# Optimization experiments

Hardware: AMD Instinct MI355X
Metric: run time of the kernel (lower is better)

Reference implementation:

```python
import jax, jax.numpy as jnp
import numpy as np

N, K, F, H, C = 16384, 16, 3, 64, 10


def setup_inputs() -> dict:
    key = jax.random.key(0)
    ks = jax.random.split(key, 6)
    pos = jax.random.normal(ks[0], (N, F), jnp.float32)
    batch = jnp.zeros((N,), jnp.int32)  # single graph
    W1 = jax.random.normal(ks[1], (2 * F, H), jnp.float32) * 0.1
    b1 = jnp.zeros((H,), jnp.float32)
    W2 = jax.random.normal(ks[2], (2 * H, H), jnp.float32) * 0.1
    b2 = jnp.zeros((H,), jnp.float32)
    Wc = jax.random.normal(ks[3], (H, C), jnp.float32) * 0.1
    bc = jnp.zeros((C,), jnp.float32)
    return {"pos": pos, "batch": batch, "W1": W1, "b1": b1,
            "W2": W2, "b2": b2, "Wc": Wc, "bc": bc}


def knn_graph(pos, k):
    # brute-force knn with self-loops (loop=True): self has distance 0
    sq = jnp.sum(pos * pos, axis=1)
    d = sq[:, None] + sq[None, :] - 2.0 * (pos @ pos.T)  # [N, N]
    _, idx = jax.lax.top_k(-d, k)  # [N, k] nearest neighbor indices (incl. self)
    return idx


def edge_conv(x, idx, W, b):
    # message for edge j->i: Linear(concat(x_i, x_j - x_i)); aggregate by max over neighbors
    n, k = idx.shape
    xi = x[:, None, :]               # [N, 1, F]
    xj = x[idx]                      # [N, k, F]
    msg = jnp.concatenate([jnp.broadcast_to(xi, (n, k, x.shape[1])), xj - xi], axis=-1)
    m = msg @ W + b                  # [N, k, H]
    return jnp.max(m, axis=1)        # [N, H]


def reference(pos, batch, W1, b1, W2, b2, Wc, bc):
    idx = knn_graph(pos, K)
    h = jax.nn.relu(edge_conv(pos, idx, W1, b1))
    h = jax.nn.relu(edge_conv(h, idx, W2, b2))
    g = jax.ops.segment_max(h, batch, num_segments=1)  # global max pool -> [1, H]
    return g @ Wc + bc
```

## Files before the change

### kernel.cpp

```cpp
#include <hip/hip_runtime.h>

#define NPTS 16384
#define KNN 16
#define HID 64
#define NCLS 10

#define CHUNKS_T 16
#define CHUNK_T (NPTS / CHUNKS_T)
#define NSTR 16
#define CHUNKS_S 32
#define CHUNK_S (NPTS / CHUNKS_S)
#define CAPS 12

__device__ __forceinline__ float distf(float4 q, float4 p) {
    float dot = fmaf(q.x, p.x, fmaf(q.y, p.y, q.z * p.z));
    return fmaf(-2.f, dot, p.w);
}

__device__ __forceinline__ unsigned long long dkey(float v, int j) {
    unsigned u = __float_as_uint(v);
    u = (u & 0x80000000u) ? ~u : (u | 0x80000000u);
    return ((unsigned long long)u << 32) | (unsigned)j;
}

__device__ __forceinline__ unsigned long long shfl_xor_u64(unsigned long long x, int m) {
    unsigned hi = (unsigned)__shfl_xor((int)(x >> 32), m, 64);
    unsigned lo = (unsigned)__shfl_xor((int)(x & 0xffffffffu), m, 64);
    return ((unsigned long long)hi << 32) | lo;
}

template <int NS>
__device__ __forceinline__ void wave_top16(unsigned long long (&key)[NS], int lane,
                                           int q, int* __restrict__ idx) {
    int outj = 0x7fffffff;
    for (int r = 0; r < 16; ++r) {
        unsigned long long gm = key[0];
#pragma unroll
        for (int s = 1; s < NS; ++s) gm = key[s] < gm ? key[s] : gm;
#pragma unroll
        for (int st = 1; st < 64; st <<= 1) {
            unsigned long long o = shfl_xor_u64(gm, st);
            gm = o < gm ? o : gm;
        }
        if (lane == r) outj = (int)(gm & 0xffffffffu);
#pragma unroll
        for (int s = 0; s < NS; ++s)
            if (key[s] == gm) key[s] = ~0ull;
    }
    if (lane < 16) idx[q * KNN + lane] = outj;
}

__global__ void prep_kernel(const float* __restrict__ pos, float4* __restrict__ pos4) {
    int i = blockIdx.x * 256 + threadIdx.x;
    if (i < NPTS) {
        float x = pos[3 * i], y = pos[3 * i + 1], z = pos[3 * i + 2];
        pos4[i] = make_float4(x, y, z, fmaf(x, x, fmaf(y, y, z * z)));
    }
}

__global__ __launch_bounds__(256) void knn_tau_kernel(const float4* __restrict__ pos4,
                                                      float* __restrict__ minpart) {
    int tid = threadIdx.x;
    int q0 = blockIdx.x * 512 + tid;
    int q1 = q0 + 256;
    int c = blockIdx.y;
    float4 qa = pos4[q0];
    float4 qb = pos4[q1];
    float mna[NSTR], mnb[NSTR];
#pragma unroll
    for (int u = 0; u < NSTR; ++u) { mna[u] = INFINITY; mnb[u] = INFINITY; }
    __shared__ float4 tile[256];
    int base = c * CHUNK_T;
    for (int t0 = 0; t0 < CHUNK_T; t0 += 256) {
        __syncthreads();
        tile[tid] = pos4[base + t0 + tid];
        __syncthreads();
        for (int jj = 0; jj < 256; jj += NSTR) {
#pragma unroll
            for (int u = 0; u < NSTR; ++u) {
                float4 p = tile[jj + u];
                mna[u] = fminf(mna[u], distf(qa, p));
                mnb[u] = fminf(mnb[u], distf(qb, p));
            }
        }
    }
#pragma unroll
    for (int u = 0; u < NSTR; ++u) {
        minpart[(c * NSTR + u) * NPTS + q0] = mna[u];
        minpart[(c * NSTR + u) * NPTS + q1] = mnb[u];
    }
}

__global__ __launch_bounds__(256) void knn_tau_reduce_kernel(const float* __restrict__ minpart,
                                                             float* __restrict__ tau) {
    int q = blockIdx.x * 256 + threadIdx.x;
    float t = -INFINITY;
#pragma unroll
    for (int u = 0; u < NSTR; ++u) {
        float m = INFINITY;
#pragma unroll
        for (int c = 0; c < CHUNKS_T; ++c) m = fminf(m, minpart[(c * NSTR + u) * NPTS + q]);
        t = fmaxf(t, m);
    }
    tau[q] = t;
}

__global__ __launch_bounds__(256) void knn_survey_kernel(const float4* __restrict__ pos4,
                                                         const float* __restrict__ tau,
                                                         int* __restrict__ surv,
                                                         int* __restrict__ cnt,
                                                         int* __restrict__ flags) {
    int tid = threadIdx.x;
    int q0 = blockIdx.x * 512 + tid;
    int q1 = q0 + 256;
    int c = blockIdx.y;
    float4 qa = pos4[q0], qb = pos4[q1];
    float ta = tau[q0], tb = tau[q1];
    __shared__ float4 tile[256];
    int base = c * CHUNK_S;
    int ca = 0, cb = 0;
    int sba = (q0 * CHUNKS_S + c) * CAPS;
    int sbb = (q1 * CHUNKS_S + c) * CAPS;
    for (int t0 = 0; t0 < CHUNK_S; t0 += 256) {
        __syncthreads();
        tile[tid] = pos4[base + t0 + tid];
        __syncthreads();
#pragma unroll 4
        for (int jj = 0; jj < 256; ++jj) {
            float4 p = tile[jj];
            int j = base + t0 + jj;
            float va = distf(qa, p);
            float vb = distf(qb, p);
            if (va <= ta) { if (ca < CAPS) surv[sba + ca] = j; ++ca; }
            if (vb <= tb) { if (cb < CAPS) surv[sbb + cb] = j; ++cb; }
        }
    }
    cnt[q0 * CHUNKS_S + c] = ca;
    cnt[q1 * CHUNKS_S + c] = cb;
    if (ca > CAPS) flags[q0] = 1;
    if (cb > CAPS) flags[q1] = 1;
}

__global__ __launch_bounds__(256) void knn_final_kernel(const float4* __restrict__ pos4,
                                                        const int* __restrict__ surv,
                                                        const int* __restrict__ cnt,
                                                        const int* __restrict__ flags,
                                                        const float* __restrict__ tau,
                                                        int* __restrict__ idx) {
    __shared__ unsigned long long buf[4][CHUNKS_S * CAPS];
    __shared__ int nbuf[4];
    int lane = threadIdx.x & 63;
    int w = threadIdx.x >> 6;
    int q = blockIdx.x * 4 + w;
    float4 qp = pos4[q];
    if (lane == 0) nbuf[w] = 0;
    if (flags[q] == 0) {
        int c = lane & 31;
        int sb = lane >> 5;
        int n = min(cnt[q * CHUNKS_S + c], CAPS);
        int sbase = (q * CHUNKS_S + c) * CAPS;
        int nv = n - sb;
        int nk = nv > 0 ? (nv + 1) >> 1 : 0;
        unsigned long long key[6];
#pragma unroll
        for (int r = 0; r < 6; ++r) key[r] = ~0ull;
#pragma unroll
        for (int r = 0; r < 6; ++r) {
            if (r < nk) {
                int j = surv[sbase + sb + 2 * r];
                key[r] = dkey(distf(qp, pos4[j]), j);
            }
        }
        int pos = atomicAdd(&nbuf[w], nk);
#pragma unroll
        for (int r = 0; r < 6; ++r)
            if (r < nk) buf[w][pos + r] = key[r];
        int ntot = atomicAdd(&nbuf[w], 0);
        int rank[6];
#pragma unroll
        for (int r = 0; r < 6; ++r) rank[r] = 0;
        for (int t = 0; t < ntot; ++t) {
            unsigned long long k = buf[w][t];
#pragma unroll
            for (int r = 0; r < 6; ++r) rank[r] += (int)(r < nk && k < key[r]);
        }
#pragma unroll
        for (int r = 0; r < 6; ++r)
            if (r < nk && rank[r] < 16) idx[q * KNN + rank[r]] = (int)(key[r] & 0xffffffffu);
    } else {
        float tq = tau[q];
        unsigned long long key[16];
#pragma unroll
        for (int u = 0; u < 16; ++u) key[u] = ~0ull;
        for (int j = lane; j < NPTS; j += 64) {
            float v = distf(qp, pos4[j]);
            unsigned long long k = dkey(v, j);
            if (v <= tq && k < key[15]) {
#pragma unroll
                for (int s = 0; s < 16; ++s) {
                    unsigned long long mn = k < key[s] ? k : key[s];
                    unsigned long long mx = k < key[s] ? key[s] : k;
                    key[s] = mn;
                    k = mx;
                }
            }
        }
        wave_top16<16>(key, lane, q, idx);
    }
}


__global__ __launch_bounds__(256) void ec1_pre_kernel(const float4* __restrict__ pos4,
                                                      const float* __restrict__ W1,
                                                      const float* __restrict__ b1,
                                                      float* __restrict__ C1,
                                                      float* __restrict__ Y1) {
    int t = threadIdx.x & 63;
    int p = blockIdx.x * 4 + (threadIdx.x >> 6);
    float4 x = pos4[p];
    float w0 = W1[0 * HID + t], w1 = W1[1 * HID + t], w2 = W1[2 * HID + t];
    float v0 = W1[3 * HID + t], v1 = W1[4 * HID + t], v2 = W1[5 * HID + t];
    float y = fmaf(x.x, v0, fmaf(x.y, v1, x.z * v2));
    float cc = b1[t] + x.x * (w0 - v0) + x.y * (w1 - v1) + x.z * (w2 - v2);
    Y1[p * HID + t] = y;
    C1[p * HID + t] = cc;
}

__global__ __launch_bounds__(256) void ec1_max_kernel(const float* __restrict__ C1,
                                                      const float* __restrict__ Y1,
                                                      const int* __restrict__ idx,
                                                      float* __restrict__ h1) {
    int t = threadIdx.x & 63;
    int p = blockIdx.x * 4 + (threadIdx.x >> 6);
    float m = -INFINITY;
#pragma unroll
    for (int k = 0; k < KNN; ++k) {
        int j = idx[p * KNN + k];
        m = fmaxf(m, Y1[j * HID + t]);
    }
    h1[p * HID + t] = fmaxf(C1[p * HID + t] + m, 0.f);
}

__global__ __launch_bounds__(256) void ec2_pre_kernel(const float* __restrict__ h1,
                                                      const float* __restrict__ W2,
                                                      const float* __restrict__ b2,
                                                      float* __restrict__ C2,
                                                      float* __restrict__ Y2) {
    int t = threadIdx.x & 63;
    int r = threadIdx.x >> 6;
    int pb = blockIdx.x * 16 + r * 4;
    float aa[4] = {0.f, 0.f, 0.f, 0.f};
    float ab[4] = {0.f, 0.f, 0.f, 0.f};
#pragma unroll 8
    for (int f = 0; f < 64; ++f) {
        float wa = W2[f * HID + t];
        float wb = W2[(64 + f) * HID + t];
#pragma unroll
        for (int i = 0; i < 4; ++i) {
            float h = h1[(pb + i) * HID + f];
            aa[i] = fmaf(h, wa, aa[i]);
            ab[i] = fmaf(h, wb, ab[i]);
        }
    }
    float bt = b2[t];
#pragma unroll
    for (int i = 0; i < 4; ++i) {
        C2[(pb + i) * HID + t] = bt + aa[i] - ab[i];
        Y2[(pb + i) * HID + t] = ab[i];
    }
}

__global__ __launch_bounds__(256) void ec2_maxpool_kernel(const float* __restrict__ C2,
                                                          const float* __restrict__ Y2,
                                                          const int* __restrict__ idx,
                                                          float* __restrict__ gpartial) {
    int t = threadIdx.x & 63;
    int lp = threadIdx.x >> 6;
    int p = blockIdx.x * 4 + lp;
    float m = -INFINITY;
#pragma unroll
    for (int k = 0; k < KNN; ++k) {
        int j = idx[p * KNN + k];
        m = fmaxf(m, Y2[j * HID + t]);
    }
    float val = fmaxf(C2[p * HID + t] + m, 0.f);
    __shared__ float red[4][64];
    red[lp][t] = val;
    __syncthreads();
    if (lp == 0) {
        float g = fmaxf(fmaxf(red[0][t], red[1][t]), fmaxf(red[2][t], red[3][t]));
        gpartial[blockIdx.x * 64 + t] = g;
    }
}

__global__ __launch_bounds__(256) void greduce2_kernel(const float* __restrict__ gpartial,
                                                       float* __restrict__ gp2) {
    __shared__ float red[4][64];
    int f = threadIdx.x & 63;
    int w = threadIdx.x >> 6;
    int r0 = blockIdx.x * 16 + w * 4;
    float m = -INFINITY;
#pragma unroll
    for (int r = 0; r < 4; ++r) m = fmaxf(m, gpartial[(r0 + r) * 64 + f]);
    red[w][f] = m;
    __syncthreads();
    if (w == 0)
        gp2[blockIdx.x * 64 + f] =
            fmaxf(fmaxf(red[0][f], red[1][f]), fmaxf(red[2][f], red[3][f]));
}

__global__ __launch_bounds__(256) void tail2_kernel(const float* __restrict__ gp2,
                                                    const float* __restrict__ Wc,
                                                    const float* __restrict__ bc,
                                                    float* __restrict__ out) {
    __shared__ float red[4][64];
    __shared__ float g[64];
    int f = threadIdx.x & 63;
    int w = threadIdx.x >> 6;
    float m = -INFINITY;
    for (int i = w; i < 256; i += 4) m = fmaxf(m, gp2[i * 64 + f]);
    red[w][f] = m;
    __syncthreads();
    if (w == 0) g[f] = fmaxf(fmaxf(red[0][f], red[1][f]), fmaxf(red[2][f], red[3][f]));
    __syncthreads();
    if (threadIdx.x < NCLS) {
        float a = bc[threadIdx.x];
#pragma unroll
        for (int h = 0; h < HID; ++h) a = fmaf(g[h], Wc[h * NCLS + threadIdx.x], a);
        out[threadIdx.x] = a;
    }
}

extern "C" void kernel_launch(void* const* d_in, const int* in_sizes, int n_in,
                              void* d_out, int out_size, void* d_ws, size_t ws_size,
                              hipStream_t stream) {
    const float* pos = (const float*)d_in[0];
    const float* W1 = (const float*)d_in[2];
    const float* b1 = (const float*)d_in[3];
    const float* W2 = (const float*)d_in[4];
    const float* b2 = (const float*)d_in[5];
    const float* Wc = (const float*)d_in[6];
    const float* bc = (const float*)d_in[7];
    float* out = (float*)d_out;

    char* ws = (char*)d_ws;
    size_t o = 0;
    auto alloc = [&](size_t bytes) { size_t r = o; o += (bytes + 255) & ~size_t(255); return r; };
    size_t sz_minp = (size_t)NPTS * CHUNKS_T * NSTR * 4;
    size_t sz_surv = (size_t)NPTS * CHUNKS_S * CAPS * 4;
    size_t o_pos4 = alloc((size_t)NPTS * 16);
    size_t o_shared = alloc(sz_minp > sz_surv ? sz_minp : sz_surv);
    size_t o_tau = alloc((size_t)NPTS * 4);
    size_t o_cnt = alloc((size_t)NPTS * CHUNKS_S * 4);
    size_t o_flag = alloc((size_t)NPTS * 4);
    size_t o_idx = alloc((size_t)NPTS * KNN * 4);
    size_t o_h1 = alloc((size_t)NPTS * HID * 4);
    size_t o_gp = alloc((size_t)(NPTS / 4) * HID * 4);
    size_t o_gp2 = alloc((size_t)256 * HID * 4);

    float4* pos4 = (float4*)(ws + o_pos4);
    float* minp = (float*)(ws + o_shared);
    int* surv = (int*)(ws + o_shared);
    size_t fm = (size_t)NPTS * HID * 4;
    float* C1 = (float*)(ws + o_shared + 0 * fm);
    float* Y1 = (float*)(ws + o_shared + 1 * fm);
    float* C2 = (float*)(ws + o_shared + 2 * fm);
    float* Y2 = (float*)(ws + o_shared + 3 * fm);
    float* tau = (float*)(ws + o_tau);
    int* cnt = (int*)(ws + o_cnt);
    int* flags = (int*)(ws + o_flag);
    int* idx = (int*)(ws + o_idx);
    float* h1 = (float*)(ws + o_h1);
    float* gp = (float*)(ws + o_gp);
    float* gp2 = (float*)(ws + o_gp2);

    hipMemsetAsync(flags, 0, (size_t)NPTS * 4, stream);

    prep_kernel<<<NPTS / 256, 256, 0, stream>>>(pos, pos4);
    knn_tau_kernel<<<dim3(NPTS / 512, CHUNKS_T), 256, 0, stream>>>(pos4, minp);
    knn_tau_reduce_kernel<<<NPTS / 256, 256, 0, stream>>>(minp, tau);
    knn_survey_kernel<<<dim3(NPTS / 512, CHUNKS_S), 256, 0, stream>>>(pos4, tau, surv, cnt, flags);
    knn_final_kernel<<<NPTS / 4, 256, 0, stream>>>(pos4, surv, cnt, flags, tau, idx);
    ec1_pre_kernel<<<NPTS / 4, 256, 0, stream>>>(pos4, W1, b1, C1, Y1);
    ec1_max_kernel<<<NPTS / 4, 256, 0, stream>>>(C1, Y1, idx, h1);
    ec2_pre_kernel<<<NPTS / 16, 256, 0, stream>>>(h1, W2, b2, C2, Y2);
    ec2_maxpool_kernel<<<NPTS / 4, 256, 0, stream>>>(C2, Y2, idx, gp);
    greduce2_kernel<<<256, 256, 0, stream>>>(gp, gp2);
    tail2_kernel<<<1, 256, 0, stream>>>(gp2, Wc, bc, out);
}
```

Measured before the change: 345.3 us.

## Store precomputed distance keys in survey and restructure survey chunking

The survey kernel now writes 64-bit distance/index keys for surviving candidates instead of bare indices, so the final kernel reads the keys directly rather than gathering neighbor positions and recomputing distances. Survey also moves to one query per thread with 16 chunks and a capacity of 16 per chunk, instead of two queries per thread with 32 chunks of capacity 12. The final kernel maps 16 chunks by 4 sub-lanes, each handling up to 4 keys. This doubles the bytes per survivor slot and changes the survey's per-thread work and grid shape. A larger per-chunk capacity may also send fewer queries to the slow fallback path.

```diff
diff --git a/kernel.cpp b/kernel.cpp
--- a/kernel.cpp
+++ b/kernel.cpp
@@ -8,9 +8,9 @@
 #define CHUNKS_T 16
 #define CHUNK_T (NPTS / CHUNKS_T)
 #define NSTR 16
-#define CHUNKS_S 32
+#define CHUNKS_S 16
 #define CHUNK_S (NPTS / CHUNKS_S)
-#define CAPS 12
+#define CAPS 16
 
 __device__ __forceinline__ float distf(float4 q, float4 p) {
     float dot = fmaf(q.x, p.x, fmaf(q.y, p.y, q.z * p.z));
@@ -107,42 +107,37 @@
 
 __global__ __launch_bounds__(256) void knn_survey_kernel(const float4* __restrict__ pos4,
                                                          const float* __restrict__ tau,
-                                                         int* __restrict__ surv,
+                                                         unsigned long long* __restrict__ surv,
                                                          int* __restrict__ cnt,
                                                          int* __restrict__ flags) {
     int tid = threadIdx.x;
-    int q0 = blockIdx.x * 512 + tid;
-    int q1 = q0 + 256;
+    int q = blockIdx.x * 256 + tid;
     int c = blockIdx.y;
-    float4 qa = pos4[q0], qb = pos4[q1];
-    float ta = tau[q0], tb = tau[q1];
+    float4 qp = pos4[q];
+    float tq = tau[q];
     __shared__ float4 tile[256];
     int base = c * CHUNK_S;
-    int ca = 0, cb = 0;
-    int sba = (q0 * CHUNKS_S + c) * CAPS;
-    int sbb = (q1 * CHUNKS_S + c) * CAPS;
+    int cr = 0;
+    int sbase = (q * CHUNKS_S + c) * CAPS;
     for (int t0 = 0; t0 < CHUNK_S; t0 += 256) {
         __syncthreads();
         tile[tid] = pos4[base + t0 + tid];
         __syncthreads();
 #pragma unroll 4
         for (int jj = 0; jj < 256; ++jj) {
-            float4 p = tile[jj];
-            int j = base + t0 + jj;
-            float va = distf(qa, p);
-            float vb = distf(qb, p);
-            if (va <= ta) { if (ca < CAPS) surv[sba + ca] = j; ++ca; }
-            if (vb <= tb) { if (cb < CAPS) surv[sbb + cb] = j; ++cb; }
-        }
-    }
-    cnt[q0 * CHUNKS_S + c] = ca;
-    cnt[q1 * CHUNKS_S + c] = cb;
-    if (ca > CAPS) flags[q0] = 1;
-    if (cb > CAPS) flags[q1] = 1;
+            float v = distf(qp, tile[jj]);
+            if (v <= tq) {
+                if (cr < CAPS) surv[sbase + cr] = dkey(v, base + t0 + jj);
+                ++cr;
+            }
+        }
+    }
+    cnt[q * CHUNKS_S + c] = cr;
+    if (cr > CAPS) flags[q] = 1;
 }
 
 __global__ __launch_bounds__(256) void knn_final_kernel(const float4* __restrict__ pos4,
-                                                        const int* __restrict__ surv,
+                                                        const unsigned long long* __restrict__ surv,
                                                         const int* __restrict__ cnt,
                                                         const int* __restrict__ flags,
                                                         const float* __restrict__ tau,
@@ -152,42 +147,36 @@
     int lane = threadIdx.x & 63;
     int w = threadIdx.x >> 6;
     int q = blockIdx.x * 4 + w;
-    float4 qp = pos4[q];
     if (lane == 0) nbuf[w] = 0;
     if (flags[q] == 0) {
-        int c = lane & 31;
-        int sb = lane >> 5;
+        int c = lane & 15;
+        int sb = lane >> 4;
         int n = min(cnt[q * CHUNKS_S + c], CAPS);
         int sbase = (q * CHUNKS_S + c) * CAPS;
         int nv = n - sb;
-        int nk = nv > 0 ? (nv + 1) >> 1 : 0;
-        unsigned long long key[6];
-#pragma unroll
-        for (int r = 0; r < 6; ++r) key[r] = ~0ull;
-#pragma unroll
-        for (int r = 0; r < 6; ++r) {
-            if (r < nk) {
-                int j = surv[sbase + sb + 2 * r];
-                key[r] = dkey(distf(qp, pos4[j]), j);
-            }
-        }
+        int nk = nv > 0 ? (nv + 3) >> 2 : 0;
+        unsigned long long key[4];
+#pragma unroll
+        for (int r = 0; r < 4; ++r)
+            key[r] = (r < nk) ? surv[sbase + sb + 4 * r] : ~0ull;
         int pos = atomicAdd(&nbuf[w], nk);
 #pragma unroll
-        for (int r = 0; r < 6; ++r)
+        for (int r = 0; r < 4; ++r)
             if (r < nk) buf[w][pos + r] = key[r];
         int ntot = atomicAdd(&nbuf[w], 0);
-        int rank[6];
-#pragma unroll
-        for (int r = 0; r < 6; ++r) rank[r] = 0;
+        int rank[4];
+#pragma unroll
+        for (int r = 0; r < 4; ++r) rank[r] = 0;
         for (int t = 0; t < ntot; ++t) {
             unsigned long long k = buf[w][t];
 #pragma unroll
-            for (int r = 0; r < 6; ++r) rank[r] += (int)(r < nk && k < key[r]);
-        }
-#pragma unroll
-        for (int r = 0; r < 6; ++r)
+            for (int r = 0; r < 4; ++r) rank[r] += (int)(r < nk && k < key[r]);
+        }
+#pragma unroll
+        for (int r = 0; r < 4; ++r)
             if (r < nk && rank[r] < 16) idx[q * KNN + rank[r]] = (int)(key[r] & 0xffffffffu);
     } else {
+        float4 qp = pos4[q];
         float tq = tau[q];
         unsigned long long key[16];
 #pragma unroll
@@ -347,7 +336,7 @@
     size_t o = 0;
     auto alloc = [&](size_t bytes) { size_t r = o; o += (bytes + 255) & ~size_t(255); return r; };
     size_t sz_minp = (size_t)NPTS * CHUNKS_T * NSTR * 4;
-    size_t sz_surv = (size_t)NPTS * CHUNKS_S * CAPS * 4;
+    size_t sz_surv = (size_t)NPTS * CHUNKS_S * CAPS * 8;
     size_t o_pos4 = alloc((size_t)NPTS * 16);
     size_t o_shared = alloc(sz_minp > sz_surv ? sz_minp : sz_surv);
     size_t o_tau = alloc((size_t)NPTS * 4);
@@ -360,7 +349,7 @@
 
     float4* pos4 = (float4*)(ws + o_pos4);
     float* minp = (float*)(ws + o_shared);
-    int* surv = (int*)(ws + o_shared);
+    unsigned long long* surv = (unsigned long long*)(ws + o_shared);
     size_t fm = (size_t)NPTS * HID * 4;
     float* C1 = (float*)(ws + o_shared + 0 * fm);
     float* Y1 = (float*)(ws + o_shared + 1 * fm);
@@ -379,7 +368,7 @@
     prep_kernel<<<NPTS / 256, 256, 0, stream>>>(pos, pos4);
     knn_tau_kernel<<<dim3(NPTS / 512, CHUNKS_T), 256, 0, stream>>>(pos4, minp);
     knn_tau_reduce_kernel<<<NPTS / 256, 256, 0, stream>>>(minp, tau);
-    knn_survey_kernel<<<dim3(NPTS / 512, CHUNKS_S), 256, 0, stream>>>(pos4, tau, surv, cnt, flags);
+    knn_survey_kernel<<<dim3(NPTS / 256, CHUNKS_S), 256, 0, stream>>>(pos4, tau, surv, cnt, flags);
     knn_final_kernel<<<NPTS / 4, 256, 0, stream>>>(pos4, surv, cnt, flags, tau, idx);
     ec1_pre_kernel<<<NPTS / 4, 256, 0, stream>>>(pos4, W1, b1, C1, Y1);
     ec1_max_kernel<<<NPTS / 4, 256, 0, stream>>>(C1, Y1, idx, h1);
```

After: 387.4 us. 12.2% more time.
